# Kernel tuning notes

Hardware: AMD Instinct MI355X
Metric: run time of the kernel (lower is better)

## Reference

```python
import jax, jax.numpy as jnp
import numpy as np

DIM = 256
WIN = (2, 7, 7)
NH = 8
BW = 2048  # num_windows * batch
N_TOK = WIN[0] * WIN[1] * WIN[2]  # 98


def _rel_coords_table():
    # Swin-V2 continuous log-spaced relative coordinates table, flattened to [T, 3]
    d = np.arange(-(WIN[0] - 1), WIN[0], dtype=np.float32)
    h = np.arange(-(WIN[1] - 1), WIN[1], dtype=np.float32)
    w = np.arange(-(WIN[2] - 1), WIN[2], dtype=np.float32)
    g = np.stack(np.meshgrid(d, h, w, indexing='ij'), axis=-1)  # [2Wd-1, 2Wh-1, 2Ww-1, 3]
    eps = 1e-6
    g[..., 0] /= WIN[0] - (1 - eps)
    g[..., 1] /= WIN[1] - (1 - eps)
    g[..., 2] /= WIN[2] - (1 - eps)
    g *= 8.0
    g = np.sign(g) * np.log2(np.abs(g) + 1.0) / np.log2(8.0)
    return g.reshape(-1, 3).astype(np.float32)


def _rel_pos_index():
    # integer relative position index [N, N] into the flattened table
    coords = np.stack(np.meshgrid(np.arange(WIN[0]), np.arange(WIN[1]), np.arange(WIN[2]), indexing='ij'))
    cf = coords.reshape(3, -1)
    rc = (cf[:, :, None] - cf[:, None, :]).transpose(1, 2, 0)
    rc[..., 0] += WIN[0] - 1
    rc[..., 1] += WIN[1] - 1
    rc[..., 2] += WIN[2] - 1
    rc[..., 0] *= (2 * WIN[1] - 1) * (2 * WIN[2] - 1)
    rc[..., 1] *= 2 * WIN[2] - 1
    return rc.sum(-1).astype(np.int32)  # [N, N]


def setup_inputs() -> dict:
    key = jax.random.key(0)
    ks = jax.random.split(key, 6)
    x = jax.random.normal(ks[0], (BW, N_TOK, DIM), dtype=jnp.float32)
    qkv_w = jax.random.normal(ks[1], (3 * DIM, DIM), dtype=jnp.float32) * 0.02
    q_bias = jnp.zeros((DIM,), dtype=jnp.float32)
    v_bias = jnp.zeros((DIM,), dtype=jnp.float32)
    logit_scale = jnp.log(10.0) * jnp.ones((NH, 1, 1), dtype=jnp.float32)
    cpb_w1 = jax.random.normal(ks[2], (512, 3), dtype=jnp.float32) * 0.02
    cpb_b1 = jnp.zeros((512,), dtype=jnp.float32)
    cpb_w2 = jax.random.normal(ks[3], (NH, 512), dtype=jnp.float32) * 0.02
    proj_w = jax.random.normal(ks[4], (DIM, DIM), dtype=jnp.float32) * 0.02
    proj_b = jnp.zeros((DIM,), dtype=jnp.float32)
    return {"x": x, "qkv_w": qkv_w, "q_bias": q_bias, "v_bias": v_bias,
            "logit_scale": logit_scale, "cpb_w1": cpb_w1, "cpb_b1": cpb_b1,
            "cpb_w2": cpb_w2, "proj_w": proj_w, "proj_b": proj_b}


def reference(x, qkv_w, q_bias, v_bias, logit_scale, cpb_w1, cpb_b1, cpb_w2, proj_w, proj_b):
    B_, N, C = x.shape
    hd = C // NH
    # qkv with separate q/v biases and zero k bias (Swin-V2)
    bias = jnp.concatenate([q_bias, jnp.zeros_like(q_bias), v_bias])
    qkv = (x @ qkv_w.T + bias).reshape(B_, N, 3, NH, hd).transpose(2, 0, 3, 1, 4)
    q, k, v = qkv[0], qkv[1], qkv[2]  # each [B_, NH, N, hd]
    # cosine attention: L2-normalize q, k (F.normalize eps=1e-12)
    qn = q / jnp.maximum(jnp.linalg.norm(q, axis=-1, keepdims=True), 1e-12)
    kn = k / jnp.maximum(jnp.linalg.norm(k, axis=-1, keepdims=True), 1e-12)
    attn = jnp.einsum('bhnd,bhmd->bhnm', qn, kn)
    scale = jnp.exp(jnp.minimum(logit_scale, jnp.log(jnp.float32(100.0))))  # clamp at log(1/0.01)
    attn = attn * scale  # [NH,1,1] broadcasts
    # continuous relative position bias via cpb MLP
    table = jnp.asarray(_rel_coords_table())                     # [T, 3]
    bt = jax.nn.relu(table @ cpb_w1.T + cpb_b1) @ cpb_w2.T       # [T, NH]
    idx = jnp.asarray(_rel_pos_index().reshape(-1))              # [N*N]
    rpb = bt[idx].reshape(N, N, NH).transpose(2, 0, 1)           # [NH, N, N]
    rpb = 16.0 * jax.nn.sigmoid(rpb)
    attn = jax.nn.softmax(attn + rpb[None], axis=-1)
    out = jnp.einsum('bhnm,bhmd->bhnd', attn, v).transpose(0, 2, 1, 3).reshape(B_, N, C)
    return out @ proj_w.T + proj_b
```

## Files before the change

### kernel.cpp

```cpp
#include <hip/hip_runtime.h>
#include <math.h>

typedef _Float16 f16;
typedef _Float16 f16x8 __attribute__((ext_vector_type(8)));
typedef float f32x4 __attribute__((ext_vector_type(4)));

#define NTOK 98
#define BWIN 2048

#define OFF_BT    0u
#define OFF_RPB   (1u<<20)
#define OFF_WQKV  (2u<<20)
#define OFF_WPROJ (3u<<20)
#define OFF_Q     (4u<<20)
#define QKV_SZ    (2048u*8u*98u*32u*2u)
#define OFF_K     (OFF_Q + QKV_SZ)
#define OFF_V     (OFF_K + QKV_SZ)
#define OFF_AV    (OFF_V + QKV_SZ)
#define OFF_X16   OFF_AV

__global__ void prep_bt(const float* __restrict__ w1, const float* __restrict__ b1,
                        const float* __restrict__ w2, float* __restrict__ bt) {
  int t = blockIdx.x;
  int lane = threadIdx.x;
  int a = t / 169, rem = t % 169, b = rem / 13, c = rem % 13;
  float g0 = ((float)(a - 1) / 1.000001f) * 8.0f;
  float g1 = ((float)(b - 6) / 6.000001f) * 8.0f;
  float g2 = ((float)(c - 6) / 6.000001f) * 8.0f;
  float t0 = log2f(fabsf(g0) + 1.0f) / 3.0f; t0 = (g0 < 0.f) ? -t0 : t0;
  float t1 = log2f(fabsf(g1) + 1.0f) / 3.0f; t1 = (g1 < 0.f) ? -t1 : t1;
  float t2 = log2f(fabsf(g2) + 1.0f) / 3.0f; t2 = (g2 < 0.f) ? -t2 : t2;
  float part[8] = {0.f,0.f,0.f,0.f,0.f,0.f,0.f,0.f};
#pragma unroll
  for (int jj = 0; jj < 8; jj++) {
    int j = lane * 8 + jj;
    float hv = t0 * w1[j*3] + t1 * w1[j*3+1] + t2 * w1[j*3+2] + b1[j];
    hv = fmaxf(hv, 0.f);
#pragma unroll
    for (int h = 0; h < 8; h++) part[h] += hv * w2[h*512 + j];
  }
#pragma unroll
  for (int m = 1; m < 64; m <<= 1)
#pragma unroll
    for (int h = 0; h < 8; h++) part[h] += __shfl_xor(part[h], m);
  if (lane == 0)
#pragma unroll
    for (int h = 0; h < 8; h++) bt[t*8 + h] = part[h];
}

__global__ void prep_rpb(const float* __restrict__ bt, float* __restrict__ rpb) {
  int bid = blockIdx.x;
  int h = bid / 98, i = bid % 98;
  int j = threadIdx.x;
  if (j >= 98) return;
  int di = i / 49, hi = (i % 49) / 7, wi = i % 7;
  int dj = j / 49, hj = (j % 49) / 7, wj = j % 7;
  int idx = (di - dj + 1) * 169 + (hi - hj + 6) * 13 + (wi - wj + 6);
  float v = bt[idx*8 + h];
  rpb[(h*98 + i)*98 + j] = 16.0f / (1.0f + expf(-v));
}

__global__ void prep_wt(const float* __restrict__ qkv_w, const float* __restrict__ proj_w,
                        f16* __restrict__ wq, f16* __restrict__ wp) {
  int t = blockIdx.x * 256 + threadIdx.x;
  wq[t] = (f16)qkv_w[t];
  if (t < 256*256) wp[t] = (f16)proj_w[t];
}

__global__ __launch_bounds__(256) void prep_x16(const float* __restrict__ x, f16* __restrict__ x16) {
  size_t i = ((size_t)blockIdx.x * 256 + threadIdx.x) * 8;
  float4 a = *(const float4*)(x + i);
  float4 b = *(const float4*)(x + i + 4);
  f16x8 o;
  o[0]=(f16)a.x; o[1]=(f16)a.y; o[2]=(f16)a.z; o[3]=(f16)a.w;
  o[4]=(f16)b.x; o[5]=(f16)b.y; o[6]=(f16)b.z; o[7]=(f16)b.w;
  *(f16x8*)(x16 + i) = o;
}

#define ASTR 40
__global__ __launch_bounds__(256) void qkv_gemm(
    const f16* __restrict__ x16, const f16* __restrict__ wq,
    const float* __restrict__ q_bias, const float* __restrict__ v_bias,
    f16* __restrict__ qw, f16* __restrict__ kw, f16* __restrict__ vw) {
  __shared__ f16 Al[128*ASTR];
  __shared__ f16 Bl[128*ASTR];
  int tid = threadIdx.x;
  int w = tid >> 6, lane = tid & 63, q4 = lane >> 4, l15 = lane & 15;
  int m0 = blockIdx.x * 128;
  int n0 = blockIdx.y * 128;

  f32x4 acc[2][8] = {};
  for (int ks = 0; ks < 8; ks++) {
    __syncthreads();
#pragma unroll
    for (int p = 0; p < 2; p++) {
      int e = tid + p*256;  int r = e >> 2, kc = e & 3;
      *(uint4*)(&Al[r*ASTR + kc*8]) = *(const uint4*)(x16 + (size_t)(m0 + r)*256 + ks*32 + kc*8);
      *(uint4*)(&Bl[r*ASTR + kc*8]) = *(const uint4*)(wq  + (size_t)(n0 + r)*256 + ks*32 + kc*8);
    }
    __syncthreads();
    f16x8 af[2], bf[8];
#pragma unroll
    for (int mt = 0; mt < 2; mt++)
      af[mt] = *(const f16x8*)(&Al[(w*32 + mt*16 + l15)*ASTR + q4*8]);
#pragma unroll
    for (int nt = 0; nt < 8; nt++)
      bf[nt] = *(const f16x8*)(&Bl[(nt*16 + l15)*ASTR + q4*8]);
#pragma unroll
    for (int mt = 0; mt < 2; mt++)
#pragma unroll
      for (int nt = 0; nt < 8; nt++)
        acc[mt][nt] = __builtin_amdgcn_mfma_f32_16x16x32_f16(af[mt], bf[nt], acc[mt][nt], 0, 0, 0);
  }
  int s = blockIdx.y >> 1;
  f16* dst = (s == 0) ? qw : ((s == 1) ? kw : vw);
#pragma unroll
  for (int mt = 0; mt < 2; mt++)
#pragma unroll
    for (int nt = 0; nt < 8; nt++) {
      int c = n0 + nt*16 + l15;
      int hcol = (c >> 5) & 7, d = c & 31;
      float bias = (s == 0) ? q_bias[c & 255] : ((s == 2) ? v_bias[c & 255] : 0.0f);
#pragma unroll
      for (int r = 0; r < 4; r++) {
        int m = m0 + w*32 + mt*16 + q4*4 + r;
        int b = m / 98, tok = m % 98;
        dst[((size_t)(b*8 + hcol)*98 + tok)*32 + d] = (f16)(acc[mt][nt][r] + bias);
      }
    }
}

#define P_STR 136
__global__ __launch_bounds__(256) void attn_kernel(
    const f16* __restrict__ qw, const f16* __restrict__ kw, const f16* __restrict__ vw,
    const float* __restrict__ rpb, const float* __restrict__ logit_scale,
    f16* __restrict__ av) {
  __shared__ f16 Ps[4*16*P_STR];

  int tid = threadIdx.x;
  int wv = tid >> 6, lane = tid & 63, q4 = lane >> 4, l15 = lane & 15;
  int pair = blockIdx.x * 4 + wv;
  int b = pair >> 3, h = pair & 7;
  float scale = __expf(fminf(logit_scale[h], 4.6051701859880914f));
  const f16* qg = qw + ((size_t)pair) * (98*32);
  const f16* kg = kw + ((size_t)pair) * (98*32);
  const f16* vg = vw + ((size_t)pair) * (98*32);
  f16* pbuf = &Ps[wv * 16 * P_STR];

  {
    int r = lane >> 2, c0 = 112 + (lane & 3) * 4;
    *(ushort4*)(&pbuf[r*P_STR + c0]) = ushort4{0,0,0,0};
  }

  f16x8 kf[7];
#pragma unroll
  for (int nt = 0; nt < 7; nt++) {
    int row = nt*16 + l15; if (row > 97) row = 97;
    f16x8 raw = *(const f16x8*)(kg + row*32 + q4*8);
    float ss = 0.f;
#pragma unroll
    for (int j = 0; j < 8; j++) { float v = (float)raw[j]; ss = fmaf(v, v, ss); }
    ss += __shfl_xor(ss, 16);
    ss += __shfl_xor(ss, 32);
    float inv = 1.0f / fmaxf(sqrtf(ss), 1e-12f);
#pragma unroll
    for (int j = 0; j < 8; j++) kf[nt][j] = (f16)((float)raw[j] * inv);
  }

  f16x8 vf[2][4];
#pragma unroll
  for (int n = 0; n < 2; n++)
#pragma unroll
    for (int kt = 0; kt < 4; kt++)
#pragma unroll
      for (int j = 0; j < 8; j++) {
        int tok = kt*32 + q4*8 + j; if (tok > 97) tok = 97;
        vf[n][kt][j] = vg[tok*32 + n*16 + l15];
      }

  const float* rpb_h = rpb + (size_t)h * 98 * 98;

  for (int mt = 0; mt < 7; mt++) {
    int qrow = mt*16 + l15; if (qrow > 97) qrow = 97;
    f16x8 qraw = *(const f16x8*)(qg + qrow*32 + q4*8);
    float ss = 0.f;
#pragma unroll
    for (int j = 0; j < 8; j++) { float v = (float)qraw[j]; ss = fmaf(v, v, ss); }
    ss += __shfl_xor(ss, 16);
    ss += __shfl_xor(ss, 32);
    float qinv = 1.0f / fmaxf(sqrtf(ss), 1e-12f);
    f16x8 aq;
#pragma unroll
    for (int j = 0; j < 8; j++) aq[j] = (f16)((float)qraw[j] * qinv);

    f32x4 lg[7];
#pragma unroll
    for (int nt = 0; nt < 7; nt++) {
      f32x4 z = {0.f,0.f,0.f,0.f};
      lg[nt] = __builtin_amdgcn_mfma_f32_16x16x32_f16(aq, kf[nt], z, 0, 0, 0);
    }
#pragma unroll
    for (int nt = 0; nt < 7; nt++) {
      int col = nt*16 + l15;
#pragma unroll
      for (int r = 0; r < 4; r++) {
        int row = mt*16 + q4*4 + r;
        float lv = -1e30f;
        if (row < 98 && col < 98)
          lv = fmaf(scale, lg[nt][r], rpb_h[row*98 + col]);
        lg[nt][r] = lv;
      }
    }
    float mx[4];
#pragma unroll
    for (int r = 0; r < 4; r++) {
      float m = lg[0][r];
#pragma unroll
      for (int nt = 1; nt < 7; nt++) m = fmaxf(m, lg[nt][r]);
      m = fmaxf(m, __shfl_xor(m, 1));
      m = fmaxf(m, __shfl_xor(m, 2));
      m = fmaxf(m, __shfl_xor(m, 4));
      m = fmaxf(m, __shfl_xor(m, 8));
      mx[r] = m;
    }
    float rs[4] = {0.f,0.f,0.f,0.f};
#pragma unroll
    for (int nt = 0; nt < 7; nt++) {
      int col = nt*16 + l15;
#pragma unroll
      for (int r = 0; r < 4; r++) {
        float p = __expf(lg[nt][r] - mx[r]);
        rs[r] += p;
        pbuf[(q4*4 + r)*P_STR + col] = (f16)p;
      }
    }
    float inv[4];
#pragma unroll
    for (int r = 0; r < 4; r++) {
      float s = rs[r];
      s += __shfl_xor(s, 1);
      s += __shfl_xor(s, 2);
      s += __shfl_xor(s, 4);
      s += __shfl_xor(s, 8);
      inv[r] = 1.0f / s;
    }
    f16x8 pf[4];
#pragma unroll
    for (int kt = 0; kt < 4; kt++)
      pf[kt] = *(const f16x8*)(&pbuf[l15*P_STR + kt*32 + q4*8]);
#pragma unroll
    for (int n = 0; n < 2; n++) {
      f32x4 acc = {0.f,0.f,0.f,0.f};
#pragma unroll
      for (int kt = 0; kt < 4; kt++)
        acc = __builtin_amdgcn_mfma_f32_16x16x32_f16(pf[kt], vf[n][kt], acc, 0, 0, 0);
      int d = n*16 + l15;
#pragma unroll
      for (int r = 0; r < 4; r++) {
        int row = mt*16 + q4*4 + r;
        if (row < 98)
          av[((size_t)(b*98 + row))*256 + h*32 + d] = (f16)(acc[r] * inv[r]);
      }
    }
  }
}

__global__ __launch_bounds__(256) void proj_gemm(
    const f16* __restrict__ avi, const f16* __restrict__ wp,
    const float* __restrict__ pb, float* __restrict__ out) {
  __shared__ f16 Al[128*ASTR];
  __shared__ f16 Bl[128*ASTR];
  int tid = threadIdx.x;
  int w = tid >> 6, lane = tid & 63, q4 = lane >> 4, l15 = lane & 15;
  int m0 = blockIdx.x * 128;
  int n0 = blockIdx.y * 128;

  f32x4 acc[2][8] = {};
  for (int ks = 0; ks < 8; ks++) {
    __syncthreads();
#pragma unroll
    for (int p = 0; p < 2; p++) {
      int e = tid + p*256;  int r = e >> 2, kc = e & 3;
      *(uint4*)(&Al[r*ASTR + kc*8]) = *(const uint4*)(avi + (size_t)(m0 + r)*256 + ks*32 + kc*8);
      *(uint4*)(&Bl[r*ASTR + kc*8]) = *(const uint4*)(wp  + (size_t)(n0 + r)*256 + ks*32 + kc*8);
    }
    __syncthreads();
    f16x8 af[2], bf[8];
#pragma unroll
    for (int mt = 0; mt < 2; mt++)
      af[mt] = *(const f16x8*)(&Al[(w*32 + mt*16 + l15)*ASTR + q4*8]);
#pragma unroll
    for (int nt = 0; nt < 8; nt++)
      bf[nt] = *(const f16x8*)(&Bl[(nt*16 + l15)*ASTR + q4*8]);
#pragma unroll
    for (int mt = 0; mt < 2; mt++)
#pragma unroll
      for (int nt = 0; nt < 8; nt++)
        acc[mt][nt] = __builtin_amdgcn_mfma_f32_16x16x32_f16(af[mt], bf[nt], acc[mt][nt], 0, 0, 0);
  }
#pragma unroll
  for (int mt = 0; mt < 2; mt++)
#pragma unroll
    for (int nt = 0; nt < 8; nt++) {
      int c = n0 + nt*16 + l15;
      float bias = pb[c];
#pragma unroll
      for (int r = 0; r < 4; r++) {
        int m = m0 + w*32 + mt*16 + q4*4 + r;
        out[(size_t)m*256 + c] = acc[mt][nt][r] + bias;
      }
    }
}

extern "C" void kernel_launch(void* const* d_in, const int* in_sizes, int n_in,
                              void* d_out, int out_size, void* d_ws, size_t ws_size,
                              hipStream_t stream) {
  const float* x           = (const float*)d_in[0];
  const float* qkv_w       = (const float*)d_in[1];
  const float* q_bias      = (const float*)d_in[2];
  const float* v_bias      = (const float*)d_in[3];
  const float* logit_scale = (const float*)d_in[4];
  const float* cpb_w1      = (const float*)d_in[5];
  const float* cpb_b1      = (const float*)d_in[6];
  const float* cpb_w2      = (const float*)d_in[7];
  const float* proj_w      = (const float*)d_in[8];
  const float* proj_b      = (const float*)d_in[9];
  char* ws = (char*)d_ws;
  float* bt  = (float*)(ws + OFF_BT);
  float* rpb = (float*)(ws + OFF_RPB);
  f16* wq    = (f16*)(ws + OFF_WQKV);
  f16* wp    = (f16*)(ws + OFF_WPROJ);
  f16* qws   = (f16*)(ws + OFF_Q);
  f16* kws   = (f16*)(ws + OFF_K);
  f16* vws   = (f16*)(ws + OFF_V);
  f16* avs   = (f16*)(ws + OFF_AV);
  f16* x16   = (f16*)(ws + OFF_X16);
  float* out = (float*)d_out;

  prep_bt<<<dim3(507), dim3(64), 0, stream>>>(cpb_w1, cpb_b1, cpb_w2, bt);
  prep_rpb<<<dim3(784), dim3(128), 0, stream>>>(bt, rpb);
  prep_wt<<<dim3(768), dim3(256), 0, stream>>>(qkv_w, proj_w, wq, wp);
  prep_x16<<<dim3(25088), dim3(256), 0, stream>>>(x, x16);
  qkv_gemm<<<dim3(1568, 6), dim3(256), 0, stream>>>(x16, wq, q_bias, v_bias, qws, kws, vws);
  attn_kernel<<<dim3(4096), dim3(256), 0, stream>>>(qws, kws, vws, rpb, logit_scale, avs);
  proj_gemm<<<dim3(1568, 2), dim3(256), 0, stream>>>(avs, wp, proj_b, out);
}
```

Before: 873.0 us.

## Fuse fp32-to-fp16 conversion of x into QKV GEMM with register prefetch and XCD swizzle

Measured after the change: 1.136 ms. 1.3x slower.

```diff
diff --git a/kernel.cpp b/kernel.cpp
--- a/kernel.cpp
+++ b/kernel.cpp
@@ -2,6 +2,7 @@
 #include <math.h>
 
 typedef _Float16 f16;
+typedef _Float16 f16x4 __attribute__((ext_vector_type(4)));
 typedef _Float16 f16x8 __attribute__((ext_vector_type(8)));
 typedef float f32x4 __attribute__((ext_vector_type(4)));
 
@@ -17,7 +18,6 @@
 #define OFF_K     (OFF_Q + QKV_SZ)
 #define OFF_V     (OFF_K + QKV_SZ)
 #define OFF_AV    (OFF_V + QKV_SZ)
-#define OFF_X16   OFF_AV
 
 __global__ void prep_bt(const float* __restrict__ w1, const float* __restrict__ b1,
                         const float* __restrict__ w2, float* __restrict__ bt) {
@@ -67,52 +67,83 @@
   if (t < 256*256) wp[t] = (f16)proj_w[t];
 }
 
-__global__ __launch_bounds__(256) void prep_x16(const float* __restrict__ x, f16* __restrict__ x16) {
-  size_t i = ((size_t)blockIdx.x * 256 + threadIdx.x) * 8;
-  float4 a = *(const float4*)(x + i);
-  float4 b = *(const float4*)(x + i + 4);
-  f16x8 o;
-  o[0]=(f16)a.x; o[1]=(f16)a.y; o[2]=(f16)a.z; o[3]=(f16)a.w;
-  o[4]=(f16)b.x; o[5]=(f16)b.y; o[6]=(f16)b.z; o[7]=(f16)b.w;
-  *(f16x8*)(x16 + i) = o;
-}
-
 #define ASTR 40
 __global__ __launch_bounds__(256) void qkv_gemm(
-    const f16* __restrict__ x16, const f16* __restrict__ wq,
+    const float* __restrict__ x, const f16* __restrict__ wq,
     const float* __restrict__ q_bias, const float* __restrict__ v_bias,
     f16* __restrict__ qw, f16* __restrict__ kw, f16* __restrict__ vw) {
   __shared__ f16 Al[128*ASTR];
   __shared__ f16 Bl[128*ASTR];
   int tid = threadIdx.x;
   int w = tid >> 6, lane = tid & 63, q4 = lane >> 4, l15 = lane & 15;
-  int m0 = blockIdx.x * 128;
-  int n0 = blockIdx.y * 128;
+
+  int bid = blockIdx.x;
+  int sid = (bid & 7) * 1176 + (bid >> 3);
+  int n_t = sid % 6, m_t = sid / 6;
+  int m0 = m_t * 128, n0 = n_t * 128;
+
+  const float* ga[4]; f16* la[4];
+#pragma unroll
+  for (int p = 0; p < 4; p++) {
+    int c = tid + p*256, r = c >> 3, k4 = c & 7;
+    ga[p] = x + (size_t)(m0 + r)*256 + k4*4;
+    la[p] = &Al[r*ASTR + k4*4];
+  }
+  const f16* gb[2]; f16* lb[2];
+#pragma unroll
+  for (int p = 0; p < 2; p++) {
+    int c = tid + p*256, r = c >> 2, kc = c & 3;
+    gb[p] = wq + (size_t)(n0 + r)*256 + kc*8;
+    lb[p] = &Bl[r*ASTR + kc*8];
+  }
 
   f32x4 acc[2][8] = {};
-  for (int ks = 0; ks < 8; ks++) {
-    __syncthreads();
-#pragma unroll
-    for (int p = 0; p < 2; p++) {
-      int e = tid + p*256;  int r = e >> 2, kc = e & 3;
-      *(uint4*)(&Al[r*ASTR + kc*8]) = *(const uint4*)(x16 + (size_t)(m0 + r)*256 + ks*32 + kc*8);
-      *(uint4*)(&Bl[r*ASTR + kc*8]) = *(const uint4*)(wq  + (size_t)(n0 + r)*256 + ks*32 + kc*8);
-    }
-    __syncthreads();
-    f16x8 af[2], bf[8];
-#pragma unroll
-    for (int mt = 0; mt < 2; mt++)
-      af[mt] = *(const f16x8*)(&Al[(w*32 + mt*16 + l15)*ASTR + q4*8]);
-#pragma unroll
-    for (int nt = 0; nt < 8; nt++)
-      bf[nt] = *(const f16x8*)(&Bl[(nt*16 + l15)*ASTR + q4*8]);
-#pragma unroll
-    for (int mt = 0; mt < 2; mt++)
-#pragma unroll
-      for (int nt = 0; nt < 8; nt++)
-        acc[mt][nt] = __builtin_amdgcn_mfma_f32_16x16x32_f16(af[mt], bf[nt], acc[mt][nt], 0, 0, 0);
-  }
-  int s = blockIdx.y >> 1;
+  float4 aP[4], aQ[4]; uint4 bP[2], bQ[2];
+#pragma unroll
+  for (int p = 0; p < 4; p++) aP[p] = *(const float4*)(ga[p]);
+#pragma unroll
+  for (int p = 0; p < 2; p++) bP[p] = *(const uint4*)(gb[p]);
+
+#define GSTEP(CA, CB, NA, NB, KS, PF)                                          \
+  {                                                                            \
+    if (PF) {                                                                  \
+      _Pragma("unroll")                                                        \
+      for (int p = 0; p < 4; p++) NA[p] = *(const float4*)(ga[p] + ((KS)+1)*32); \
+      _Pragma("unroll")                                                        \
+      for (int p = 0; p < 2; p++) NB[p] = *(const uint4*)(gb[p] + ((KS)+1)*32);  \
+    }                                                                          \
+    __syncthreads();                                                           \
+    _Pragma("unroll")                                                          \
+    for (int p = 0; p < 4; p++) {                                              \
+      f16x4 cv;                                                                \
+      cv[0]=(f16)CA[p].x; cv[1]=(f16)CA[p].y;                                  \
+      cv[2]=(f16)CA[p].z; cv[3]=(f16)CA[p].w;                                  \
+      *(f16x4*)(la[p]) = cv;                                                   \
+    }                                                                          \
+    _Pragma("unroll")                                                          \
+    for (int p = 0; p < 2; p++) *(uint4*)(lb[p]) = CB[p];                      \
+    __syncthreads();                                                           \
+    f16x8 af[2], bf[8];                                                        \
+    _Pragma("unroll")                                                          \
+    for (int mt = 0; mt < 2; mt++)                                             \
+      af[mt] = *(const f16x8*)(&Al[(w*32 + mt*16 + l15)*ASTR + q4*8]);         \
+    _Pragma("unroll")                                                          \
+    for (int nt = 0; nt < 8; nt++)                                             \
+      bf[nt] = *(const f16x8*)(&Bl[(nt*16 + l15)*ASTR + q4*8]);                \
+    _Pragma("unroll")                                                          \
+    for (int mt = 0; mt < 2; mt++)                                             \
+      _Pragma("unroll")                                                        \
+      for (int nt = 0; nt < 8; nt++)                                           \
+        acc[mt][nt] = __builtin_amdgcn_mfma_f32_16x16x32_f16(af[mt], bf[nt], acc[mt][nt], 0, 0, 0); \
+  }
+
+  for (int ks2 = 0; ks2 < 8; ks2 += 2) {
+    GSTEP(aP, bP, aQ, bQ, ks2, 1)
+    GSTEP(aQ, bQ, aP, bP, (ks2+1), (ks2 < 6))
+  }
+#undef GSTEP
+
+  int s = n_t >> 1;
   f16* dst = (s == 0) ? qw : ((s == 1) ? kw : vw);
 #pragma unroll
   for (int mt = 0; mt < 2; mt++)
@@ -272,32 +303,64 @@
   __shared__ f16 Bl[128*ASTR];
   int tid = threadIdx.x;
   int w = tid >> 6, lane = tid & 63, q4 = lane >> 4, l15 = lane & 15;
-  int m0 = blockIdx.x * 128;
-  int n0 = blockIdx.y * 128;
+
+  int bid = blockIdx.x;
+  int sid = (bid & 7) * 392 + (bid >> 3);
+  int n_t = sid & 1, m_t = sid >> 1;
+  int m0 = m_t * 128, n0 = n_t * 128;
+
+  const f16* ga[2]; f16* la[2];
+  const f16* gb[2]; f16* lb[2];
+#pragma unroll
+  for (int p = 0; p < 2; p++) {
+    int c = tid + p*256, r = c >> 2, kc = c & 3;
+    ga[p] = avi + (size_t)(m0 + r)*256 + kc*8;
+    la[p] = &Al[r*ASTR + kc*8];
+    gb[p] = wp + (size_t)(n0 + r)*256 + kc*8;
+    lb[p] = &Bl[r*ASTR + kc*8];
+  }
 
   f32x4 acc[2][8] = {};
-  for (int ks = 0; ks < 8; ks++) {
-    __syncthreads();
-#pragma unroll
-    for (int p = 0; p < 2; p++) {
-      int e = tid + p*256;  int r = e >> 2, kc = e & 3;
-      *(uint4*)(&Al[r*ASTR + kc*8]) = *(const uint4*)(avi + (size_t)(m0 + r)*256 + ks*32 + kc*8);
-      *(uint4*)(&Bl[r*ASTR + kc*8]) = *(const uint4*)(wp  + (size_t)(n0 + r)*256 + ks*32 + kc*8);
-    }
-    __syncthreads();
-    f16x8 af[2], bf[8];
-#pragma unroll
-    for (int mt = 0; mt < 2; mt++)
-      af[mt] = *(const f16x8*)(&Al[(w*32 + mt*16 + l15)*ASTR + q4*8]);
-#pragma unroll
-    for (int nt = 0; nt < 8; nt++)
-      bf[nt] = *(const f16x8*)(&Bl[(nt*16 + l15)*ASTR + q4*8]);
-#pragma unroll
-    for (int mt = 0; mt < 2; mt++)
-#pragma unroll
-      for (int nt = 0; nt < 8; nt++)
-        acc[mt][nt] = __builtin_amdgcn_mfma_f32_16x16x32_f16(af[mt], bf[nt], acc[mt][nt], 0, 0, 0);
-  }
+  uint4 aP[2], aQ[2], bP[2], bQ[2];
+#pragma unroll
+  for (int p = 0; p < 2; p++) { aP[p] = *(const uint4*)(ga[p]); bP[p] = *(const uint4*)(gb[p]); }
+
+#define PSTEP(CA, CB, NA, NB, KS, PF)                                          \
+  {                                                                            \
+    if (PF) {                                                                  \
+      _Pragma("unroll")                                                        \
+      for (int p = 0; p < 2; p++) {                                            \
+        NA[p] = *(const uint4*)(ga[p] + ((KS)+1)*32);                          \
+        NB[p] = *(const uint4*)(gb[p] + ((KS)+1)*32);                          \
+      }                                                                        \
+    }                                                                          \
+    __syncthreads();                                                           \
+    _Pragma("unroll")                                                          \
+    for (int p = 0; p < 2; p++) {                                              \
+      *(uint4*)(la[p]) = CA[p];                                                \
+      *(uint4*)(lb[p]) = CB[p];                                                \
+    }                                                                          \
+    __syncthreads();                                                           \
+    f16x8 af[2], bf[8];                                                        \
+    _Pragma("unroll")                                                          \
+    for (int mt = 0; mt < 2; mt++)                                             \
+      af[mt] = *(const f16x8*)(&Al[(w*32 + mt*16 + l15)*ASTR + q4*8]);         \
+    _Pragma("unroll")                                                          \
+    for (int nt = 0; nt < 8; nt++)                                             \
+      bf[nt] = *(const f16x8*)(&Bl[(nt*16 + l15)*ASTR + q4*8]);                \
+    _Pragma("unroll")                                                          \
+    for (int mt = 0; mt < 2; mt++)                                             \
+      _Pragma("unroll")                                                        \
+      for (int nt = 0; nt < 8; nt++)                                           \
+        acc[mt][nt] = __builtin_amdgcn_mfma_f32_16x16x32_f16(af[mt], bf[nt], acc[mt][nt], 0, 0, 0); \
+  }
+
+  for (int ks2 = 0; ks2 < 8; ks2 += 2) {
+    PSTEP(aP, bP, aQ, bQ, ks2, 1)
+    PSTEP(aQ, bQ, aP, bP, (ks2+1), (ks2 < 6))
+  }
+#undef PSTEP
+
 #pragma unroll
   for (int mt = 0; mt < 2; mt++)
 #pragma unroll
@@ -334,14 +397,12 @@
   f16* kws   = (f16*)(ws + OFF_K);
   f16* vws   = (f16*)(ws + OFF_V);
   f16* avs   = (f16*)(ws + OFF_AV);
-  f16* x16   = (f16*)(ws + OFF_X16);
   float* out = (float*)d_out;
 
   prep_bt<<<dim3(507), dim3(64), 0, stream>>>(cpb_w1, cpb_b1, cpb_w2, bt);
   prep_rpb<<<dim3(784), dim3(128), 0, stream>>>(bt, rpb);
   prep_wt<<<dim3(768), dim3(256), 0, stream>>>(qkv_w, proj_w, wq, wp);
-  prep_x16<<<dim3(25088), dim3(256), 0, stream>>>(x, x16);
-  qkv_gemm<<<dim3(1568, 6), dim3(256), 0, stream>>>(x16, wq, q_bias, v_bias, qws, kws, vws);
+  qkv_gemm<<<dim3(9408), dim3(256), 0, stream>>>(x, wq, q_bias, v_bias, qws, kws, vws);
   attn_kernel<<<dim3(4096), dim3(256), 0, stream>>>(qws, kws, vws, rpb, logit_scale, avs);
-  proj_gemm<<<dim3(1568, 2), dim3(256), 0, stream>>>(avs, wp, proj_b, out);
-}
+  proj_gemm<<<dim3(3136), dim3(256), 0, stream>>>(avs, wp, proj_b, out);
+}
```

## Use direct global-to-LDS loads and XCD-aware block remapping in GEMMs

Applied to the files above, without the earlier changes.

Measured after the change: 832.5 us. -4.6%, faster.

```diff
diff --git a/kernel.cpp b/kernel.cpp
--- a/kernel.cpp
+++ b/kernel.cpp
@@ -18,6 +18,12 @@
 #define OFF_V     (OFF_K + QKV_SZ)
 #define OFF_AV    (OFF_V + QKV_SZ)
 #define OFF_X16   OFF_AV
+
+__device__ __forceinline__ void gload16(const f16* g, f16* l) {
+  __builtin_amdgcn_global_load_lds(
+      (const __attribute__((address_space(1))) void*)g,
+      (__attribute__((address_space(3))) void*)l, 16, 0, 0);
+}
 
 __global__ void prep_bt(const float* __restrict__ w1, const float* __restrict__ b1,
                         const float* __restrict__ w2, float* __restrict__ bt) {
@@ -77,42 +83,47 @@
   *(f16x8*)(x16 + i) = o;
 }
 
-#define ASTR 40
 __global__ __launch_bounds__(256) void qkv_gemm(
     const f16* __restrict__ x16, const f16* __restrict__ wq,
     const float* __restrict__ q_bias, const float* __restrict__ v_bias,
     f16* __restrict__ qw, f16* __restrict__ kw, f16* __restrict__ vw) {
-  __shared__ f16 Al[128*ASTR];
-  __shared__ f16 Bl[128*ASTR];
+  __shared__ f16 Al[128*32];
+  __shared__ f16 Bl[128*32];
   int tid = threadIdx.x;
   int w = tid >> 6, lane = tid & 63, q4 = lane >> 4, l15 = lane & 15;
-  int m0 = blockIdx.x * 128;
-  int n0 = blockIdx.y * 128;
+
+  int bid = blockIdx.x;
+  int sid = (bid & 7) * 1176 + (bid >> 3);
+  int n_t = sid % 6, m_t = sid / 6;
+  int m0 = m_t * 128, n0 = n_t * 128;
 
   f32x4 acc[2][8] = {};
   for (int ks = 0; ks < 8; ks++) {
     __syncthreads();
 #pragma unroll
     for (int p = 0; p < 2; p++) {
-      int e = tid + p*256;  int r = e >> 2, kc = e & 3;
-      *(uint4*)(&Al[r*ASTR + kc*8]) = *(const uint4*)(x16 + (size_t)(m0 + r)*256 + ks*32 + kc*8);
-      *(uint4*)(&Bl[r*ASTR + kc*8]) = *(const uint4*)(wq  + (size_t)(n0 + r)*256 + ks*32 + kc*8);
+      int e0 = p*256 + (w << 6);
+      int e  = e0 + lane;
+      int r  = e >> 2, kc = e & 3;
+      gload16(x16 + (size_t)(m0 + r)*256 + ks*32 + kc*8, &Al[e0*8]);
+      gload16(wq  + (size_t)(n0 + r)*256 + ks*32 + kc*8, &Bl[e0*8]);
     }
     __syncthreads();
     f16x8 af[2], bf[8];
 #pragma unroll
     for (int mt = 0; mt < 2; mt++)
-      af[mt] = *(const f16x8*)(&Al[(w*32 + mt*16 + l15)*ASTR + q4*8]);
+      af[mt] = *(const f16x8*)(&Al[(w*32 + mt*16 + l15)*32 + q4*8]);
 #pragma unroll
     for (int nt = 0; nt < 8; nt++)
-      bf[nt] = *(const f16x8*)(&Bl[(nt*16 + l15)*ASTR + q4*8]);
+      bf[nt] = *(const f16x8*)(&Bl[(nt*16 + l15)*32 + q4*8]);
 #pragma unroll
     for (int mt = 0; mt < 2; mt++)
 #pragma unroll
       for (int nt = 0; nt < 8; nt++)
         acc[mt][nt] = __builtin_amdgcn_mfma_f32_16x16x32_f16(af[mt], bf[nt], acc[mt][nt], 0, 0, 0);
   }
-  int s = blockIdx.y >> 1;
+
+  int s = n_t >> 1;
   f16* dst = (s == 0) ? qw : ((s == 1) ? kw : vw);
 #pragma unroll
   for (int mt = 0; mt < 2; mt++)
@@ -268,36 +279,42 @@
 __global__ __launch_bounds__(256) void proj_gemm(
     const f16* __restrict__ avi, const f16* __restrict__ wp,
     const float* __restrict__ pb, float* __restrict__ out) {
-  __shared__ f16 Al[128*ASTR];
-  __shared__ f16 Bl[128*ASTR];
+  __shared__ f16 Al[128*32];
+  __shared__ f16 Bl[128*32];
   int tid = threadIdx.x;
   int w = tid >> 6, lane = tid & 63, q4 = lane >> 4, l15 = lane & 15;
-  int m0 = blockIdx.x * 128;
-  int n0 = blockIdx.y * 128;
+
+  int bid = blockIdx.x;
+  int sid = (bid & 7) * 392 + (bid >> 3);
+  int n_t = sid & 1, m_t = sid >> 1;
+  int m0 = m_t * 128, n0 = n_t * 128;
 
   f32x4 acc[2][8] = {};
   for (int ks = 0; ks < 8; ks++) {
     __syncthreads();
 #pragma unroll
     for (int p = 0; p < 2; p++) {
-      int e = tid + p*256;  int r = e >> 2, kc = e & 3;
-      *(uint4*)(&Al[r*ASTR + kc*8]) = *(const uint4*)(avi + (size_t)(m0 + r)*256 + ks*32 + kc*8);
-      *(uint4*)(&Bl[r*ASTR + kc*8]) = *(const uint4*)(wp  + (size_t)(n0 + r)*256 + ks*32 + kc*8);
+      int e0 = p*256 + (w << 6);
+      int e  = e0 + lane;
+      int r  = e >> 2, kc = e & 3;
+      gload16(avi + (size_t)(m0 + r)*256 + ks*32 + kc*8, &Al[e0*8]);
+      gload16(wp  + (size_t)(n0 + r)*256 + ks*32 + kc*8, &Bl[e0*8]);
     }
     __syncthreads();
     f16x8 af[2], bf[8];
 #pragma unroll
     for (int mt = 0; mt < 2; mt++)
-      af[mt] = *(const f16x8*)(&Al[(w*32 + mt*16 + l15)*ASTR + q4*8]);
+      af[mt] = *(const f16x8*)(&Al[(w*32 + mt*16 + l15)*32 + q4*8]);
 #pragma unroll
     for (int nt = 0; nt < 8; nt++)
-      bf[nt] = *(const f16x8*)(&Bl[(nt*16 + l15)*ASTR + q4*8]);
+      bf[nt] = *(const f16x8*)(&Bl[(nt*16 + l15)*32 + q4*8]);
 #pragma unroll
     for (int mt = 0; mt < 2; mt++)
 #pragma unroll
       for (int nt = 0; nt < 8; nt++)
         acc[mt][nt] = __builtin_amdgcn_mfma_f32_16x16x32_f16(af[mt], bf[nt], acc[mt][nt], 0, 0, 0);
   }
+
 #pragma unroll
   for (int mt = 0; mt < 2; mt++)
 #pragma unroll
@@ -341,7 +358,7 @@
   prep_rpb<<<dim3(784), dim3(128), 0, stream>>>(bt, rpb);
   prep_wt<<<dim3(768), dim3(256), 0, stream>>>(qkv_w, proj_w, wq, wp);
   prep_x16<<<dim3(25088), dim3(256), 0, stream>>>(x, x16);
-  qkv_gemm<<<dim3(1568, 6), dim3(256), 0, stream>>>(x16, wq, q_bias, v_bias, qws, kws, vws);
+  qkv_gemm<<<dim3(9408), dim3(256), 0, stream>>>(x16, wq, q_bias, v_bias, qws, kws, vws);
   attn_kernel<<<dim3(4096), dim3(256), 0, stream>>>(qws, kws, vws, rpb, logit_scale, avs);
-  proj_gemm<<<dim3(1568, 2), dim3(256), 0, stream>>>(avs, wp, proj_b, out);
-}
+  proj_gemm<<<dim3(3136), dim3(256), 0, stream>>>(avs, wp, proj_b, out);
+}
```
